# Optimization experiments

Measured on AMD Instinct MI355X. Metric: run time of the kernel, lower is better.

The kernel has to match this reference:

```python
import jax, jax.numpy as jnp
import numpy as np

B = 8192   # batch
N = 1024   # input feature dim
D = 64     # rotation dimension
K = D * (D - 1) // 2  # 2016 upper-triangular entries


def setup_inputs() -> dict:
    key = jax.random.key(0)
    k1, k2 = jax.random.split(key, 2)
    x = jax.random.normal(k1, (B, N), dtype=jnp.float32)
    # nn.Linear(N, K) parameters (kaiming-uniform-ish scale)
    W = jax.random.normal(k2, (K, N), dtype=jnp.float32) / np.float32(np.sqrt(N))
    b = jnp.zeros((K,), dtype=jnp.float32)
    return {"x": x, "W": W, "b": b}


def _skew_expm(A):
    # A is real skew-symmetric => iA is Hermitian: iA = V diag(w) V^H, w real.
    # Hence expm(A) = V diag(exp(-i w)) V^H, which is real orthogonal.
    # Mathematically identical to torch.linalg.matrix_exp(A).
    w, V = jnp.linalg.eigh(1j * A)              # complex64 eigh, batched
    R = jnp.einsum('bij,bj,bkj->bik', V, jnp.exp(-1j * w), V.conj())
    return jnp.real(R)


def reference(x, W, b):
    v = jax.nn.silu(x) @ W.T + b                # (B, K)
    iu, ju = jnp.triu_indices(D, k=1)           # strict upper triangle
    A = jnp.zeros((x.shape[0], D, D), v.dtype)
    A = A.at[:, iu, ju].set(v)
    A = A.at[:, ju, iu].set(-v)                 # skew-symmetric
    return _skew_expm(A)                        # (B, D, D)
```

## Files before the change

### kernel.cpp

```cpp
#include <hip/hip_runtime.h>
#include <hip/hip_bf16.h>
#include <hip/hip_fp16.h>
#include <math.h>

#define BB 8192
#define NF 1024
#define KKc 2016
#define DD 64

typedef unsigned short u16;
typedef __attribute__((ext_vector_type(4))) float f32x4;
typedef __attribute__((ext_vector_type(4))) unsigned int u32x4;
typedef __attribute__((ext_vector_type(8))) short s16x8;
typedef __attribute__((ext_vector_type(8))) _Float16 f16x8;
typedef __attribute__((ext_vector_type(8))) unsigned short u16x8;

union BF2U { __hip_bfloat162 b; unsigned u; };
union H2U { __half2 h; unsigned u; };
union F16U { s16x8 s; f16x8 h; };

__device__ __forceinline__ unsigned pk_hi(float a, float b, float& fa, float& fb) {
  BF2U r; r.b = __float22bfloat162_rn(make_float2(a, b));
  float2 f = __bfloat1622float2(r.b);
  fa = f.x; fb = f.y;
  return r.u;
}
__device__ __forceinline__ unsigned pk(float a, float b) {
  BF2U r; r.b = __float22bfloat162_rn(make_float2(a, b));
  return r.u;
}
__device__ __forceinline__ unsigned pkh(float a, float b) {
  H2U r; r.h = __float22half2_rn(make_float2(a, b));
  return r.u;
}

__device__ __forceinline__ void split4(const float t0, const float t1, const float t2,
                                       const float t3, uint2& h, uint2& l) {
  float f0, f1, f2, f3;
  h.x = pk_hi(t0, t1, f0, f1);
  h.y = pk_hi(t2, t3, f2, f3);
  l.x = pk(t0 - f0, t1 - f1);
  l.y = pk(t2 - f2, t3 - f3);
}

__global__ __launch_bounds__(256)
void prep_f16_kernel(const float* __restrict__ x, const float* __restrict__ W,
                     u16* __restrict__ xf, u16* __restrict__ wfp) {
  const int bid = blockIdx.x;
  if (bid < BB) {
    const int idx = bid * 256 + threadIdx.x;
    float4 vv = ((const float4*)x)[idx];
    float a[4] = {vv.x, vv.y, vv.z, vv.w};
#pragma unroll
    for (int i = 0; i < 4; i++) a[i] = a[i] / (1.f + __expf(-a[i]));
    uint2 o;
    o.x = pkh(a[0], a[1]);
    o.y = pkh(a[2], a[3]);
    ((uint2*)xf)[idx] = o;
  } else {
    const int idx = (bid - BB) * 256 + threadIdx.x;
    const int row = idx >> 8;
    float4 vv = make_float4(0.f, 0.f, 0.f, 0.f);
    if (row < KKc) vv = ((const float4*)W)[idx];
    uint2 o;
    o.x = pkh(vv.x, vv.y);
    o.y = pkh(vv.z, vv.w);
    ((uint2*)wfp)[idx] = o;
  }
}

typedef __attribute__((address_space(1))) const unsigned int gu32;
typedef __attribute__((address_space(3))) unsigned int lu32;

__device__ __forceinline__ void gload_lds16(const void* g, void* l) {
  __builtin_amdgcn_global_load_lds((gu32*)g, (lu32*)l, 16, 0, 0);
}

__device__ __forceinline__ s16x8 frag_row32(const u16* T, int row, int kc) {
  const int c = kc ^ ((row >> 1) & 3);
  return *(const s16x8*)(T + row * 32 + c * 8);
}

__global__ __launch_bounds__(256, 4)
void gemm_f16_kernel(const u16* __restrict__ xf, const u16* __restrict__ wfp,
                     const float* __restrict__ bias, float* __restrict__ v) {
  __shared__ __align__(16) u16 Af[128 * 32];
  __shared__ __align__(16) u16 Bf[128 * 32];
  const int tid = threadIdx.x;
  const int l = tid & 63, w = tid >> 6;
  const int wi = w >> 1, wj = w & 1;
  const int lin = (blockIdx.x & 7) * 128 + (blockIdx.x >> 3);
  const int n0 = (lin & 15) * 128;
  const int m0 = (lin >> 4) * 128;
  const int kc = l >> 4, lr = l & 15;

  const u16* P = (w < 2) ? xf : wfp;
  u16* T = (w < 2) ? Af : Bf;
  const int row0 = ((w < 2) ? m0 : n0) + (w & 1) * 64;
  u16* Th = T + (w & 1) * 2048;

  f32x4 acc[4][4];
  const f32x4 zz = {0.f, 0.f, 0.f, 0.f};
#pragma unroll
  for (int a = 0; a < 4; a++)
#pragma unroll
    for (int b = 0; b < 4; b++) acc[a][b] = zz;

  for (int k0 = 0; k0 < NF; k0 += 32) {
#pragma unroll
    for (int c4 = 0; c4 < 4; c4++) {
      const int slot = c4 * 64 + l;
      const int r = slot >> 2;
      const int c = (slot & 3) ^ ((r >> 1) & 3);
      gload_lds16(P + (size_t)(row0 + r) * NF + k0 + c * 8, Th + c4 * 512);
    }
    __syncthreads();

    F16U fa[4], fb[4];
#pragma unroll
    for (int a = 0; a < 4; a++) fa[a].s = frag_row32(Af, wi * 64 + a * 16 + lr, kc);
#pragma unroll
    for (int b = 0; b < 4; b++) fb[b].s = frag_row32(Bf, wj * 64 + b * 16 + lr, kc);
#pragma unroll
    for (int b = 0; b < 4; b++)
#pragma unroll
      for (int a = 0; a < 4; a++)
        acc[a][b] = __builtin_amdgcn_mfma_f32_16x16x32_f16(fa[a].h, fb[b].h, acc[a][b], 0, 0, 0);
    __syncthreads();
  }

  const int grp = l >> 4;
#pragma unroll
  for (int b = 0; b < 4; b++) {
    const int n = n0 + wj * 64 + b * 16 + lr;
    if (n < KKc) {
      const float bb = bias[n];
#pragma unroll
      for (int a = 0; a < 4; a++) {
        const int mbase = m0 + wi * 64 + a * 16 + grp * 4;
#pragma unroll
        for (int i = 0; i < 4; i++)
          v[(size_t)(mbase + i) * KKc + n] = acc[a][b][i] + bb;
      }
    }
  }
}

#define BM 128
#define BN 128
#define BKr 16
#define XST 132

__global__ __launch_bounds__(256, 2)
void gemm_silu_kernel(const float* __restrict__ x, const float* __restrict__ W,
                      const float* __restrict__ bias, float* __restrict__ v) {
  __shared__ float xs[BKr * XST];
  __shared__ float wl[BKr * XST];
  const int tid = threadIdx.x;
  const int tx = tid & 15, ty = tid >> 4;
  const int c0g = blockIdx.x * BN;
  const int m0 = blockIdx.y * BM;
  const int lrow = tid >> 2;
  const int lu = (tid & 3) << 2;

  float acc[2][2][4][4];
#pragma unroll
  for (int a = 0; a < 2; a++)
#pragma unroll
    for (int b = 0; b < 2; b++)
#pragma unroll
      for (int i = 0; i < 4; i++)
#pragma unroll
        for (int j = 0; j < 4; j++) acc[a][b][i][j] = 0.f;

  for (int n0 = 0; n0 < NF; n0 += BKr) {
#pragma unroll
    for (int p = 0; p < 2; p++) {
      const int row = lrow + 64 * p;
      float4 xv = *(const float4*)(x + (size_t)(m0 + row) * NF + n0 + lu);
      float xa[4] = {xv.x, xv.y, xv.z, xv.w};
#pragma unroll
      for (int u = 0; u < 4; u++) {
        const float val = xa[u];
        xs[(lu + u) * XST + row] = val / (1.f + __expf(-val));
      }
      const int wr = c0g + row;
      float4 wv = make_float4(0.f, 0.f, 0.f, 0.f);
      if (wr < KKc) wv = *(const float4*)(W + (size_t)wr * NF + n0 + lu);
      float wa[4] = {wv.x, wv.y, wv.z, wv.w};
#pragma unroll
      for (int u = 0; u < 4; u++) wl[(lu + u) * XST + row] = wa[u];
    }
    __syncthreads();
#pragma unroll
    for (int k0 = 0; k0 < BKr; k0 += 4) {
#pragma unroll
      for (int kk = 0; kk < 4; kk++) {
        const float* xr = xs + (k0 + kk) * XST;
        const float* wr_ = wl + (k0 + kk) * XST;
        float4 t;
        t = *(const float4*)(xr + 4 * ty);       float a0[4] = {t.x, t.y, t.z, t.w};
        t = *(const float4*)(xr + 64 + 4 * ty);  float a1[4] = {t.x, t.y, t.z, t.w};
        t = *(const float4*)(wr_ + 4 * tx);      float b0[4] = {t.x, t.y, t.z, t.w};
        t = *(const float4*)(wr_ + 64 + 4 * tx); float b1[4] = {t.x, t.y, t.z, t.w};
#pragma unroll
        for (int i = 0; i < 4; i++)
#pragma unroll
          for (int j = 0; j < 4; j++) {
            acc[0][0][i][j] = fmaf(a0[i], b0[j], acc[0][0][i][j]);
            acc[0][1][i][j] = fmaf(a0[i], b1[j], acc[0][1][i][j]);
            acc[1][0][i][j] = fmaf(a1[i], b0[j], acc[1][0][i][j]);
            acc[1][1][i][j] = fmaf(a1[i], b1[j], acc[1][1][i][j]);
          }
      }
    }
    __syncthreads();
  }
#pragma unroll
  for (int rb = 0; rb < 2; rb++)
#pragma unroll
    for (int ii = 0; ii < 4; ii++) {
      const int row = m0 + rb * 64 + 4 * ty + ii;
#pragma unroll
      for (int cb = 0; cb < 2; cb++) {
        const int c = c0g + cb * 64 + 4 * tx;
        if (c < KKc) {
          float4 bb = *(const float4*)(bias + c);
          float4 o;
          o.x = acc[rb][cb][ii][0] + bb.x;
          o.y = acc[rb][cb][ii][1] + bb.y;
          o.z = acc[rb][cb][ii][2] + bb.z;
          o.w = acc[rb][cb][ii][3] + bb.w;
          *(float4*)(v + (size_t)row * KKc + c) = o;
        }
      }
    }
}


__device__ __forceinline__ s16x8 fragld(const u16* P, int row, int chunk) {
  return *(const s16x8*)(P + ((row << 6) | ((chunk ^ (row & 7)) << 3)));
}

__device__ __forceinline__ void mat_mm3(const u16* APh, const u16* APl,
                                        const u16* BPh, const u16* BPl,
                                        f32x4 acc[2][2], int wi, int wj, int g, int lr) {
#pragma unroll
  for (int kb = 0; kb < 2; kb++) {
    const int ch = (kb << 2) | g;
    s16x8 bh[2], bl[2];
#pragma unroll
    for (int b = 0; b < 2; b++) {
      const int n = wj * 32 + b * 16 + lr;
      bh[b] = fragld(BPh, n, ch);
      bl[b] = fragld(BPl, n, ch);
    }
#pragma unroll
    for (int a = 0; a < 2; a++) {
      const int r = wi * 32 + a * 16 + lr;
      const s16x8 ah = fragld(APh, r, ch);
      const s16x8 al = fragld(APl, r, ch);
#pragma unroll
      for (int b = 0; b < 2; b++) {
        acc[a][b] = __builtin_amdgcn_mfma_f32_16x16x32_bf16(ah, bh[b], acc[a][b], 0, 0, 0);
        acc[a][b] = __builtin_amdgcn_mfma_f32_16x16x32_bf16(ah, bl[b], acc[a][b], 0, 0, 0);
        acc[a][b] = __builtin_amdgcn_mfma_f32_16x16x32_bf16(al, bh[b], acc[a][b], 0, 0, 0);
      }
    }
  }
}

__device__ __forceinline__ void mat_mm1h(const u16* AP, const u16* BP,
                                         f32x4 acc[2][2], int wi, int wj, int g, int lr) {
#pragma unroll
  for (int kb = 0; kb < 2; kb++) {
    const int ch = (kb << 2) | g;
    F16U bh[2];
#pragma unroll
    for (int b = 0; b < 2; b++) bh[b].s = fragld(BP, wj * 32 + b * 16 + lr, ch);
#pragma unroll
    for (int a = 0; a < 2; a++) {
      F16U ah; ah.s = fragld(AP, wi * 32 + a * 16 + lr, ch);
#pragma unroll
      for (int b = 0; b < 2; b++)
        acc[a][b] = __builtin_amdgcn_mfma_f32_16x16x32_f16(ah.h, bh[b].h, acc[a][b], 0, 0, 0);
    }
  }
}

__device__ __forceinline__ void pack_col(u16* Ch, u16* Cl, const f32x4 acc[2][2],
                                         int wi, int wj, int g, int lr) {
#pragma unroll
  for (int a = 0; a < 2; a++) {
    const int r0 = wi * 32 + a * 16 + g * 4;
#pragma unroll
    for (int b = 0; b < 2; b++) {
      const int c = wj * 32 + b * 16 + lr;
      uint2 h, l;
      split4(acc[a][b][0], acc[a][b][1], acc[a][b][2], acc[a][b][3], h, l);
      const int ad = (c << 6) | (((((r0 >> 3)) ^ (c & 7)) << 3) | (r0 & 7));
      *(uint2*)(Ch + ad) = h;
      *(uint2*)(Cl + ad) = l;
    }
  }
}

__device__ __forceinline__ void pack_colh(u16* C, const f32x4 acc[2][2], float sc,
                                          int wi, int wj, int g, int lr) {
#pragma unroll
  for (int a = 0; a < 2; a++) {
    const int r0 = wi * 32 + a * 16 + g * 4;
#pragma unroll
    for (int b = 0; b < 2; b++) {
      const int c = wj * 32 + b * 16 + lr;
      uint2 h;
      h.x = pkh(sc * acc[a][b][0], sc * acc[a][b][1]);
      h.y = pkh(sc * acc[a][b][2], sc * acc[a][b][3]);
      const int ad = (c << 6) | (((((r0 >> 3)) ^ (c & 7)) << 3) | (r0 & 7));
      *(uint2*)(C + ad) = h;
    }
  }
}

__device__ __forceinline__ void pack_dualh(u16* Rrow, u16* Rcol, const f32x4 acc[2][2],
                                           int wi, int wj, int g, int lr) {
#pragma unroll
  for (int a = 0; a < 2; a++) {
    const int r0 = wi * 32 + a * 16 + g * 4;
#pragma unroll
    for (int b = 0; b < 2; b++) {
      const int c = wj * 32 + b * 16 + lr;
      uint2 h;
      h.x = pkh(acc[a][b][0], acc[a][b][1]);
      h.y = pkh(acc[a][b][2], acc[a][b][3]);
      const int adc = (c << 6) | (((((r0 >> 3)) ^ (c & 7)) << 3) | (r0 & 7));
      *(uint2*)(Rcol + adc) = h;
      const u16 hv[4] = {(u16)h.x, (u16)(h.x >> 16), (u16)h.y, (u16)(h.y >> 16)};
#pragma unroll
      for (int i = 0; i < 4; i++) {
        const int r = r0 + i;
        const int adr = (r << 6) | ((((c >> 3) ^ (r & 7)) << 3) | (c & 7));
        Rrow[adr] = hv[i];
      }
    }
  }
}

__global__ __launch_bounds__(256, 4)
void expm_kernel(const float* __restrict__ v, float* __restrict__ out) {
  __shared__ __align__(16) u16 P0[4096], P1[4096];
  __shared__ __align__(16) u16 P2[4096], P3[4096];
  __shared__ float red[4];
  const int tid = threadIdx.x;
  const int bid = blockIdx.x;
  const int l = tid & 63, w = tid >> 6;
  const int g = l >> 4, lr = l & 15;
  const int wi = w >> 1, wj = w & 1;

  {
    const float* vr = v + (size_t)bid * KKc;
    const int arow = tid >> 2, q = tid & 3;
    const int ub = (arow * (127 - arow)) / 2 - arow - 1;
    const int c0 = q * 16;
    int il = (c0 * (127 - c0)) / 2 + arow - c0 - 1;
    float va[16];
#pragma unroll
    for (int j = 0; j < 16; j++) {
      const int c = c0 + j;
      float val = 0.f;
      if (arow < c)      val =  vr[ub + c];
      else if (arow > c) val = -vr[il];
      va[j] = val;
      il += 62 - c;
    }
#pragma unroll
    for (int cc = 0; cc < 2; cc++) {
      const int ch = 2 * q + cc;
      const int ad = (arow << 6) | ((ch ^ (arow & 7)) << 3);
      unsigned hw[4], lw[4], fw[4];
#pragma unroll
      for (int p = 0; p < 4; p++) {
        const float a = va[cc * 8 + 2 * p], b = va[cc * 8 + 2 * p + 1];
        float fa, fb;
        hw[p] = pk_hi(a, b, fa, fb);
        lw[p] = pk(a - fa, b - fb);
        fw[p] = pkh(a, b);
      }
      *(u32x4*)(P0 + ad) = (u32x4){hw[0], hw[1], hw[2], hw[3]};
      *(u32x4*)(P1 + ad) = (u32x4){lw[0], lw[1], lw[2], lw[3]};
      *(u32x4*)(P3 + ad) = (u32x4){fw[0], fw[1], fw[2], fw[3]};
    }
  }
  __syncthreads();

  const f32x4 zz = {0.f, 0.f, 0.f, 0.f};
  f32x4 acc[2][2];

  acc[0][0] = zz; acc[0][1] = zz; acc[1][0] = zz; acc[1][1] = zz;
  mat_mm1h(P3, P3, acc, wi, wj, g, lr);
  f32x4 rM[2][2];
  rM[0][0] = acc[0][0]; rM[0][1] = acc[0][1]; rM[1][0] = acc[1][0]; rM[1][1] = acc[1][1];
  pack_colh(P2, rM, -0.0625f, wi, wj, g, lr);
  __syncthreads();

  acc[0][0] = zz; acc[0][1] = zz; acc[1][0] = zz; acc[1][1] = zz;
  mat_mm1h(P2, P2, acc, wi, wj, g, lr);
  {
    float fs = 0.f;
#pragma unroll
    for (int a = 0; a < 2; a++)
#pragma unroll
      for (int b = 0; b < 2; b++)
#pragma unroll
        for (int i = 0; i < 4; i++) fs = fmaf(acc[a][b][i], acc[a][b][i], fs);
#pragma unroll
    for (int k = 1; k < 64; k <<= 1) fs += __shfl_xor(fs, k, 64);
    if (l == 0) red[w] = fs;
  }
  pack_colh(P3, acc, 1.f, wi, wj, g, lr);
  __syncthreads();

  const float nf8 = red[0] + red[1] + red[2] + red[3];
  int s = 0;
  if (nf8 > 1e-30f) {
    s = (int)ceilf(1.0f + 0.125f * log2f(nf8));
    if (s < 0) s = 0;
    if (s > 15) s = 15;
  }
  const float t = exp2f(-(float)s);
  const float t2 = t * t, t4 = t2 * t2, t6 = t4 * t2, t8 = t4 * t4;
  const float e2 = 0.5f * t2,            e4 = 256.f * t4 / 24.f;
  const float e6 = 4096.f * t6 / 720.f,  e8 = 65536.f * t8 / 40320.f;
  const float o1 = t,                    o3 = t * t2 / 6.f;
  const float o5 = 256.f * t * t4 / 120.f, o7 = 4096.f * t * t6 / 5040.f;
  const float o9 = 65536.f * t * t8 / 362880.f;

  f32x4 rE[2][2], rS3[2][2];
#pragma unroll
  for (int a = 0; a < 2; a++)
#pragma unroll
    for (int b = 0; b < 2; b++)
#pragma unroll
      for (int i = 0; i < 4; i++) {
        const int row = wi * 32 + a * 16 + g * 4 + i;
        const int col = wj * 32 + b * 16 + lr;
        const float dg = (row == col) ? 1.f : 0.f;
        rE[a][b][i]  = dg - e2 * rM[a][b][i] + e4 * acc[a][b][i];
        rS3[a][b][i] = o1 * dg - o3 * rM[a][b][i] + o5 * acc[a][b][i];
      }

  acc[0][0] = zz; acc[0][1] = zz; acc[1][0] = zz; acc[1][1] = zz;
  mat_mm1h(P3, P2, acc, wi, wj, g, lr);
#pragma unroll
  for (int a = 0; a < 2; a++)
#pragma unroll
    for (int b = 0; b < 2; b++)
#pragma unroll
      for (int i = 0; i < 4; i++) {
        rE[a][b][i]  += e6 * acc[a][b][i];
        rS3[a][b][i] += o7 * acc[a][b][i];
      }
  acc[0][0] = zz; acc[0][1] = zz; acc[1][0] = zz; acc[1][1] = zz;
  mat_mm1h(P3, P3, acc, wi, wj, g, lr);
#pragma unroll
  for (int a = 0; a < 2; a++)
#pragma unroll
    for (int b = 0; b < 2; b++)
#pragma unroll
      for (int i = 0; i < 4; i++) {
        rE[a][b][i]  += e8 * acc[a][b][i];
        rS3[a][b][i] += o9 * acc[a][b][i];
      }
  __syncthreads();

  pack_col(P2, P3, rS3, wi, wj, g, lr);
  __syncthreads();

  acc[0][0] = rE[0][0]; acc[0][1] = rE[0][1]; acc[1][0] = rE[1][0]; acc[1][1] = rE[1][1];
  mat_mm3(P0, P1, P2, P3, acc, wi, wj, g, lr);
  __syncthreads();

  for (int it = 0; it < s; it++) {
    u16* Rrow = (it & 1) ? P3 : P1;
    u16* Rcol = (it & 1) ? P2 : P0;
    pack_dualh(Rrow, Rcol, acc, wi, wj, g, lr);
    __syncthreads();
    acc[0][0] = zz; acc[0][1] = zz; acc[1][0] = zz; acc[1][1] = zz;
    mat_mm1h(Rrow, Rcol, acc, wi, wj, g, lr);
  }

  float* ob = out + (size_t)bid * 4096;
#pragma unroll
  for (int a = 0; a < 2; a++)
#pragma unroll
    for (int b = 0; b < 2; b++)
#pragma unroll
      for (int i = 0; i < 4; i++) {
        const int row = wi * 32 + a * 16 + g * 4 + i;
        const int col = wj * 32 + b * 16 + lr;
        ob[row * 64 + col] = acc[a][b][i];
      }
}

extern "C" void kernel_launch(void* const* d_in, const int* in_sizes, int n_in,
                              void* d_out, int out_size, void* d_ws, size_t ws_size,
                              hipStream_t stream) {
  const float* x = (const float*)d_in[0];
  const float* W = (const float*)d_in[1];
  const float* bias = (const float*)d_in[2];
  float* out = (float*)d_out;
  char* ws = (char*)d_ws;
  float* v = (float*)ws;

  const size_t V_BYTES  = (size_t)BB * KKc * 4;
  const size_t XF_ELEMS = (size_t)BB * NF;
  const size_t WF_ELEMS = (size_t)2048 * NF;
  const size_t NEED = V_BYTES + (XF_ELEMS + WF_ELEMS) * 2;

  if (ws_size >= NEED) {
    u16* xf = (u16*)(ws + V_BYTES);
    u16* wfp = xf + XF_ELEMS;
    prep_f16_kernel<<<dim3(BB + 2048), dim3(256), 0, stream>>>(x, W, xf, wfp);
    gemm_f16_kernel<<<dim3(1024), dim3(256), 0, stream>>>(xf, wfp, bias, v);
  } else {
    dim3 g1((KKc + BN - 1) / BN, BB / BM);
    gemm_silu_kernel<<<g1, dim3(256), 0, stream>>>(x, W, bias, v);
  }
  expm_kernel<<<dim3(BB), dim3(256), 0, stream>>>(v, out);
}
```

Measured before the change: 167.1 us.

## Track matrix and its transpose during squaring to vectorize stores

The squaring phase now keeps both R and its transpose in registers, each computed by its own MFMA product. This replaces the scattered scalar row-layout LDS writes with column-packed vector writes. Storing the transposed accumulator lets the final output go out as float4 stores instead of scalar ones. The cost is roughly double the matrix multiplies per squaring step (the last step skips one) and more register pressure.

```diff
diff --git a/kernel.cpp b/kernel.cpp
--- a/kernel.cpp
+++ b/kernel.cpp
@@ -322,30 +322,6 @@
   }
 }
 
-__device__ __forceinline__ void pack_dualh(u16* Rrow, u16* Rcol, const f32x4 acc[2][2],
-                                           int wi, int wj, int g, int lr) {
-#pragma unroll
-  for (int a = 0; a < 2; a++) {
-    const int r0 = wi * 32 + a * 16 + g * 4;
-#pragma unroll
-    for (int b = 0; b < 2; b++) {
-      const int c = wj * 32 + b * 16 + lr;
-      uint2 h;
-      h.x = pkh(acc[a][b][0], acc[a][b][1]);
-      h.y = pkh(acc[a][b][2], acc[a][b][3]);
-      const int adc = (c << 6) | (((((r0 >> 3)) ^ (c & 7)) << 3) | (r0 & 7));
-      *(uint2*)(Rcol + adc) = h;
-      const u16 hv[4] = {(u16)h.x, (u16)(h.x >> 16), (u16)h.y, (u16)(h.y >> 16)};
-#pragma unroll
-      for (int i = 0; i < 4; i++) {
-        const int r = r0 + i;
-        const int adr = (r << 6) | ((((c >> 3) ^ (r & 7)) << 3) | (c & 7));
-        Rrow[adr] = hv[i];
-      }
-    }
-  }
-}
-
 __global__ __launch_bounds__(256, 4)
 void expm_kernel(const float* __restrict__ v, float* __restrict__ out) {
   __shared__ __align__(16) u16 P0[4096], P1[4096];
@@ -476,30 +452,38 @@
   pack_col(P2, P3, rS3, wi, wj, g, lr);
   __syncthreads();
 
+  f32x4 accT[2][2];
   acc[0][0] = rE[0][0]; acc[0][1] = rE[0][1]; acc[1][0] = rE[1][0]; acc[1][1] = rE[1][1];
+  accT[0][0] = rE[0][0]; accT[0][1] = rE[0][1]; accT[1][0] = rE[1][0]; accT[1][1] = rE[1][1];
   mat_mm3(P0, P1, P2, P3, acc, wi, wj, g, lr);
+  mat_mm3(P2, P3, P0, P1, accT, wi, wj, g, lr);
   __syncthreads();
 
   for (int it = 0; it < s; it++) {
-    u16* Rrow = (it & 1) ? P3 : P1;
-    u16* Rcol = (it & 1) ? P2 : P0;
-    pack_dualh(Rrow, Rcol, acc, wi, wj, g, lr);
+    u16* Pcol = (it & 1) ? P2 : P0;
+    u16* Prow = (it & 1) ? P3 : P1;
+    pack_colh(Pcol, acc, 1.f, wi, wj, g, lr);
+    pack_colh(Prow, accT, 1.f, wi, wj, g, lr);
     __syncthreads();
-    acc[0][0] = zz; acc[0][1] = zz; acc[1][0] = zz; acc[1][1] = zz;
-    mat_mm1h(Rrow, Rcol, acc, wi, wj, g, lr);
+    accT[0][0] = zz; accT[0][1] = zz; accT[1][0] = zz; accT[1][1] = zz;
+    mat_mm1h(Pcol, Prow, accT, wi, wj, g, lr);
+    if (it < s - 1) {
+      acc[0][0] = zz; acc[0][1] = zz; acc[1][0] = zz; acc[1][1] = zz;
+      mat_mm1h(Prow, Pcol, acc, wi, wj, g, lr);
+    }
   }
 
   float* ob = out + (size_t)bid * 4096;
 #pragma unroll
-  for (int a = 0; a < 2; a++)
-#pragma unroll
-    for (int b = 0; b < 2; b++)
-#pragma unroll
-      for (int i = 0; i < 4; i++) {
-        const int row = wi * 32 + a * 16 + g * 4 + i;
-        const int col = wj * 32 + b * 16 + lr;
-        ob[row * 64 + col] = acc[a][b][i];
-      }
+  for (int a = 0; a < 2; a++) {
+    const int rt0 = wi * 32 + a * 16 + g * 4;
+#pragma unroll
+    for (int b = 0; b < 2; b++) {
+      const int ct = wj * 32 + b * 16 + lr;
+      *(float4*)(ob + ct * 64 + rt0) =
+          make_float4(accT[a][b][0], accT[a][b][1], accT[a][b][2], accT[a][b][3]);
+    }
+  }
 }
 
 extern "C" void kernel_launch(void* const* d_in, const int* in_sizes, int n_in,
```

Result: slower. 175.3 us (+4.9%).

## Split expm work across eight waves per matrix instead of four

Applied to the files above, without the earlier changes.

The expm kernel now launches 512 threads per 64x64 matrix, and each wave owns a 16x32 output tile instead of 32x32. All MFMA helpers, the pack routines, the load stage and the norm reduction are rewritten for two accumulators per wave. The aim is more waves to hide LDS and MFMA latency and fewer registers per thread. In exchange, each wave reuses its fragments less, so LDS fragment loads per MFMA rise, and block-wide barriers now synchronise more waves.

```diff
diff --git a/kernel.cpp b/kernel.cpp
--- a/kernel.cpp
+++ b/kernel.cpp
@@ -244,113 +244,93 @@
 
 __device__ __forceinline__ void mat_mm3(const u16* APh, const u16* APl,
                                         const u16* BPh, const u16* BPl,
-                                        f32x4 acc[2][2], int wi, int wj, int g, int lr) {
+                                        f32x4 acc[2], int wi, int wj, int g, int lr) {
 #pragma unroll
   for (int kb = 0; kb < 2; kb++) {
     const int ch = (kb << 2) | g;
-    s16x8 bh[2], bl[2];
+    const int r = wi * 16 + lr;
+    const s16x8 ah = fragld(APh, r, ch);
+    const s16x8 al = fragld(APl, r, ch);
 #pragma unroll
     for (int b = 0; b < 2; b++) {
       const int n = wj * 32 + b * 16 + lr;
-      bh[b] = fragld(BPh, n, ch);
-      bl[b] = fragld(BPl, n, ch);
-    }
-#pragma unroll
-    for (int a = 0; a < 2; a++) {
-      const int r = wi * 32 + a * 16 + lr;
-      const s16x8 ah = fragld(APh, r, ch);
-      const s16x8 al = fragld(APl, r, ch);
-#pragma unroll
-      for (int b = 0; b < 2; b++) {
-        acc[a][b] = __builtin_amdgcn_mfma_f32_16x16x32_bf16(ah, bh[b], acc[a][b], 0, 0, 0);
-        acc[a][b] = __builtin_amdgcn_mfma_f32_16x16x32_bf16(ah, bl[b], acc[a][b], 0, 0, 0);
-        acc[a][b] = __builtin_amdgcn_mfma_f32_16x16x32_bf16(al, bh[b], acc[a][b], 0, 0, 0);
-      }
+      const s16x8 bh = fragld(BPh, n, ch);
+      const s16x8 bl = fragld(BPl, n, ch);
+      acc[b] = __builtin_amdgcn_mfma_f32_16x16x32_bf16(ah, bh, acc[b], 0, 0, 0);
+      acc[b] = __builtin_amdgcn_mfma_f32_16x16x32_bf16(ah, bl, acc[b], 0, 0, 0);
+      acc[b] = __builtin_amdgcn_mfma_f32_16x16x32_bf16(al, bh, acc[b], 0, 0, 0);
     }
   }
 }
 
 __device__ __forceinline__ void mat_mm1h(const u16* AP, const u16* BP,
-                                         f32x4 acc[2][2], int wi, int wj, int g, int lr) {
+                                         f32x4 acc[2], int wi, int wj, int g, int lr) {
 #pragma unroll
   for (int kb = 0; kb < 2; kb++) {
     const int ch = (kb << 2) | g;
-    F16U bh[2];
-#pragma unroll
-    for (int b = 0; b < 2; b++) bh[b].s = fragld(BP, wj * 32 + b * 16 + lr, ch);
-#pragma unroll
-    for (int a = 0; a < 2; a++) {
-      F16U ah; ah.s = fragld(AP, wi * 32 + a * 16 + lr, ch);
-#pragma unroll
-      for (int b = 0; b < 2; b++)
-        acc[a][b] = __builtin_amdgcn_mfma_f32_16x16x32_f16(ah.h, bh[b].h, acc[a][b], 0, 0, 0);
-    }
-  }
-}
-
-__device__ __forceinline__ void pack_col(u16* Ch, u16* Cl, const f32x4 acc[2][2],
+    F16U ah; ah.s = fragld(AP, wi * 16 + lr, ch);
+#pragma unroll
+    for (int b = 0; b < 2; b++) {
+      F16U bh; bh.s = fragld(BP, wj * 32 + b * 16 + lr, ch);
+      acc[b] = __builtin_amdgcn_mfma_f32_16x16x32_f16(ah.h, bh.h, acc[b], 0, 0, 0);
+    }
+  }
+}
+
+__device__ __forceinline__ void pack_col(u16* Ch, u16* Cl, const f32x4 acc[2],
                                          int wi, int wj, int g, int lr) {
-#pragma unroll
-  for (int a = 0; a < 2; a++) {
-    const int r0 = wi * 32 + a * 16 + g * 4;
-#pragma unroll
-    for (int b = 0; b < 2; b++) {
-      const int c = wj * 32 + b * 16 + lr;
-      uint2 h, l;
-      split4(acc[a][b][0], acc[a][b][1], acc[a][b][2], acc[a][b][3], h, l);
-      const int ad = (c << 6) | (((((r0 >> 3)) ^ (c & 7)) << 3) | (r0 & 7));
-      *(uint2*)(Ch + ad) = h;
-      *(uint2*)(Cl + ad) = l;
-    }
-  }
-}
-
-__device__ __forceinline__ void pack_colh(u16* C, const f32x4 acc[2][2], float sc,
+  const int r0 = wi * 16 + g * 4;
+#pragma unroll
+  for (int b = 0; b < 2; b++) {
+    const int c = wj * 32 + b * 16 + lr;
+    uint2 h, l;
+    split4(acc[b][0], acc[b][1], acc[b][2], acc[b][3], h, l);
+    const int ad = (c << 6) | (((((r0 >> 3)) ^ (c & 7)) << 3) | (r0 & 7));
+    *(uint2*)(Ch + ad) = h;
+    *(uint2*)(Cl + ad) = l;
+  }
+}
+
+__device__ __forceinline__ void pack_colh(u16* C, const f32x4 acc[2], float sc,
                                           int wi, int wj, int g, int lr) {
-#pragma unroll
-  for (int a = 0; a < 2; a++) {
-    const int r0 = wi * 32 + a * 16 + g * 4;
-#pragma unroll
-    for (int b = 0; b < 2; b++) {
-      const int c = wj * 32 + b * 16 + lr;
-      uint2 h;
-      h.x = pkh(sc * acc[a][b][0], sc * acc[a][b][1]);
-      h.y = pkh(sc * acc[a][b][2], sc * acc[a][b][3]);
-      const int ad = (c << 6) | (((((r0 >> 3)) ^ (c & 7)) << 3) | (r0 & 7));
-      *(uint2*)(C + ad) = h;
-    }
-  }
-}
-
-__device__ __forceinline__ void pack_dualh(u16* Rrow, u16* Rcol, const f32x4 acc[2][2],
+  const int r0 = wi * 16 + g * 4;
+#pragma unroll
+  for (int b = 0; b < 2; b++) {
+    const int c = wj * 32 + b * 16 + lr;
+    uint2 h;
+    h.x = pkh(sc * acc[b][0], sc * acc[b][1]);
+    h.y = pkh(sc * acc[b][2], sc * acc[b][3]);
+    const int ad = (c << 6) | (((((r0 >> 3)) ^ (c & 7)) << 3) | (r0 & 7));
+    *(uint2*)(C + ad) = h;
+  }
+}
+
+__device__ __forceinline__ void pack_dualh(u16* Rrow, u16* Rcol, const f32x4 acc[2],
                                            int wi, int wj, int g, int lr) {
-#pragma unroll
-  for (int a = 0; a < 2; a++) {
-    const int r0 = wi * 32 + a * 16 + g * 4;
-#pragma unroll
-    for (int b = 0; b < 2; b++) {
-      const int c = wj * 32 + b * 16 + lr;
-      uint2 h;
-      h.x = pkh(acc[a][b][0], acc[a][b][1]);
-      h.y = pkh(acc[a][b][2], acc[a][b][3]);
-      const int adc = (c << 6) | (((((r0 >> 3)) ^ (c & 7)) << 3) | (r0 & 7));
-      *(uint2*)(Rcol + adc) = h;
-      const u16 hv[4] = {(u16)h.x, (u16)(h.x >> 16), (u16)h.y, (u16)(h.y >> 16)};
-#pragma unroll
-      for (int i = 0; i < 4; i++) {
-        const int r = r0 + i;
-        const int adr = (r << 6) | ((((c >> 3) ^ (r & 7)) << 3) | (c & 7));
-        Rrow[adr] = hv[i];
-      }
-    }
-  }
-}
-
-__global__ __launch_bounds__(256, 4)
+  const int r0 = wi * 16 + g * 4;
+#pragma unroll
+  for (int b = 0; b < 2; b++) {
+    const int c = wj * 32 + b * 16 + lr;
+    uint2 h;
+    h.x = pkh(acc[b][0], acc[b][1]);
+    h.y = pkh(acc[b][2], acc[b][3]);
+    const int adc = (c << 6) | (((((r0 >> 3)) ^ (c & 7)) << 3) | (r0 & 7));
+    *(uint2*)(Rcol + adc) = h;
+    const u16 hv[4] = {(u16)h.x, (u16)(h.x >> 16), (u16)h.y, (u16)(h.y >> 16)};
+#pragma unroll
+    for (int i = 0; i < 4; i++) {
+      const int r = r0 + i;
+      const int adr = (r << 6) | ((((c >> 3) ^ (r & 7)) << 3) | (c & 7));
+      Rrow[adr] = hv[i];
+    }
+  }
+}
+
+__global__ __launch_bounds__(512, 8)
 void expm_kernel(const float* __restrict__ v, float* __restrict__ out) {
   __shared__ __align__(16) u16 P0[4096], P1[4096];
   __shared__ __align__(16) u16 P2[4096], P3[4096];
-  __shared__ float red[4];
+  __shared__ float red[8];
   const int tid = threadIdx.x;
   const int bid = blockIdx.x;
   const int l = tid & 63, w = tid >> 6;
@@ -359,13 +339,13 @@
 
   {
     const float* vr = v + (size_t)bid * KKc;
-    const int arow = tid >> 2, q = tid & 3;
+    const int arow = tid >> 3, q = tid & 7;
     const int ub = (arow * (127 - arow)) / 2 - arow - 1;
-    const int c0 = q * 16;
+    const int c0 = q * 8;
     int il = (c0 * (127 - c0)) / 2 + arow - c0 - 1;
-    float va[16];
-#pragma unroll
-    for (int j = 0; j < 16; j++) {
+    float va[8];
+#pragma unroll
+    for (int j = 0; j < 8; j++) {
       const int c = c0 + j;
       float val = 0.f;
       if (arow < c)      val =  vr[ub + c];
@@ -373,46 +353,40 @@
       va[j] = val;
       il += 62 - c;
     }
-#pragma unroll
-    for (int cc = 0; cc < 2; cc++) {
-      const int ch = 2 * q + cc;
-      const int ad = (arow << 6) | ((ch ^ (arow & 7)) << 3);
-      unsigned hw[4], lw[4], fw[4];
-#pragma unroll
-      for (int p = 0; p < 4; p++) {
-        const float a = va[cc * 8 + 2 * p], b = va[cc * 8 + 2 * p + 1];
-        float fa, fb;
-        hw[p] = pk_hi(a, b, fa, fb);
-        lw[p] = pk(a - fa, b - fb);
-        fw[p] = pkh(a, b);
-      }
-      *(u32x4*)(P0 + ad) = (u32x4){hw[0], hw[1], hw[2], hw[3]};
-      *(u32x4*)(P1 + ad) = (u32x4){lw[0], lw[1], lw[2], lw[3]};
-      *(u32x4*)(P3 + ad) = (u32x4){fw[0], fw[1], fw[2], fw[3]};
-    }
+    const int ad = (arow << 6) | ((q ^ (arow & 7)) << 3);
+    unsigned hw[4], lw[4], fw[4];
+#pragma unroll
+    for (int p = 0; p < 4; p++) {
+      const float a = va[2 * p], b = va[2 * p + 1];
+      float fa, fb;
+      hw[p] = pk_hi(a, b, fa, fb);
+      lw[p] = pk(a - fa, b - fb);
+      fw[p] = pkh(a, b);
+    }
+    *(u32x4*)(P0 + ad) = (u32x4){hw[0], hw[1], hw[2], hw[3]};
+    *(u32x4*)(P1 + ad) = (u32x4){lw[0], lw[1], lw[2], lw[3]};
+    *(u32x4*)(P3 + ad) = (u32x4){fw[0], fw[1], fw[2], fw[3]};
   }
   __syncthreads();
 
   const f32x4 zz = {0.f, 0.f, 0.f, 0.f};
-  f32x4 acc[2][2];
-
-  acc[0][0] = zz; acc[0][1] = zz; acc[1][0] = zz; acc[1][1] = zz;
+  f32x4 acc[2];
+
+  acc[0] = zz; acc[1] = zz;
   mat_mm1h(P3, P3, acc, wi, wj, g, lr);
-  f32x4 rM[2][2];
-  rM[0][0] = acc[0][0]; rM[0][1] = acc[0][1]; rM[1][0] = acc[1][0]; rM[1][1] = acc[1][1];
+  f32x4 rM[2];
+  rM[0] = acc[0]; rM[1] = acc[1];
   pack_colh(P2, rM, -0.0625f, wi, wj, g, lr);
   __syncthreads();
 
-  acc[0][0] = zz; acc[0][1] = zz; acc[1][0] = zz; acc[1][1] = zz;
+  acc[0] = zz; acc[1] = zz;
   mat_mm1h(P2, P2, acc, wi, wj, g, lr);
   {
     float fs = 0.f;
 #pragma unroll
-    for (int a = 0; a < 2; a++)
-#pragma unroll
-      for (int b = 0; b < 2; b++)
-#pragma unroll
-        for (int i = 0; i < 4; i++) fs = fmaf(acc[a][b][i], acc[a][b][i], fs);
+    for (int b = 0; b < 2; b++)
+#pragma unroll
+      for (int i = 0; i < 4; i++) fs = fmaf(acc[b][i], acc[b][i], fs);
 #pragma unroll
     for (int k = 1; k < 64; k <<= 1) fs += __shfl_xor(fs, k, 64);
     if (l == 0) red[w] = fs;
@@ -420,7 +394,7 @@
   pack_colh(P3, acc, 1.f, wi, wj, g, lr);
   __syncthreads();
 
-  const float nf8 = red[0] + red[1] + red[2] + red[3];
+  const float nf8 = red[0] + red[1] + red[2] + red[3] + red[4] + red[5] + red[6] + red[7];
   int s = 0;
   if (nf8 > 1e-30f) {
     s = (int)ceilf(1.0f + 0.125f * log2f(nf8));
@@ -435,48 +409,42 @@
   const float o5 = 256.f * t * t4 / 120.f, o7 = 4096.f * t * t6 / 5040.f;
   const float o9 = 65536.f * t * t8 / 362880.f;
 
-  f32x4 rE[2][2], rS3[2][2];
-#pragma unroll
-  for (int a = 0; a < 2; a++)
-#pragma unroll
-    for (int b = 0; b < 2; b++)
-#pragma unroll
-      for (int i = 0; i < 4; i++) {
-        const int row = wi * 32 + a * 16 + g * 4 + i;
-        const int col = wj * 32 + b * 16 + lr;
-        const float dg = (row == col) ? 1.f : 0.f;
-        rE[a][b][i]  = dg - e2 * rM[a][b][i] + e4 * acc[a][b][i];
-        rS3[a][b][i] = o1 * dg - o3 * rM[a][b][i] + o5 * acc[a][b][i];
-      }
-
-  acc[0][0] = zz; acc[0][1] = zz; acc[1][0] = zz; acc[1][1] = zz;
+  f32x4 rE[2], rS3[2];
+#pragma unroll
+  for (int b = 0; b < 2; b++)
+#pragma unroll
+    for (int i = 0; i < 4; i++) {
+      const int row = wi * 16 + g * 4 + i;
+      const int col = wj * 32 + b * 16 + lr;
+      const float dg = (row == col) ? 1.f : 0.f;
+      rE[b][i]  = dg - e2 * rM[b][i] + e4 * acc[b][i];
+      rS3[b][i] = o1 * dg - o3 * rM[b][i] + o5 * acc[b][i];
+    }
+
+  acc[0] = zz; acc[1] = zz;
   mat_mm1h(P3, P2, acc, wi, wj, g, lr);
 #pragma unroll
-  for (int a = 0; a < 2; a++)
-#pragma unroll
-    for (int b = 0; b < 2; b++)
-#pragma unroll
-      for (int i = 0; i < 4; i++) {
-        rE[a][b][i]  += e6 * acc[a][b][i];
-        rS3[a][b][i] += o7 * acc[a][b][i];
-      }
-  acc[0][0] = zz; acc[0][1] = zz; acc[1][0] = zz; acc[1][1] = zz;
+  for (int b = 0; b < 2; b++)
+#pragma unroll
+    for (int i = 0; i < 4; i++) {
+      rE[b][i]  += e6 * acc[b][i];
+      rS3[b][i] += o7 * acc[b][i];
+    }
+  acc[0] = zz; acc[1] = zz;
   mat_mm1h(P3, P3, acc, wi, wj, g, lr);
 #pragma unroll
-  for (int a = 0; a < 2; a++)
-#pragma unroll
-    for (int b = 0; b < 2; b++)
-#pragma unroll
-      for (int i = 0; i < 4; i++) {
-        rE[a][b][i]  += e8 * acc[a][b][i];
-        rS3[a][b][i] += o9 * acc[a][b][i];
-      }
+  for (int b = 0; b < 2; b++)
+#pragma unroll
+    for (int i = 0; i < 4; i++) {
+      rE[b][i]  += e8 * acc[b][i];
+      rS3[b][i] += o9 * acc[b][i];
+    }
   __syncthreads();
 
   pack_col(P2, P3, rS3, wi, wj, g, lr);
   __syncthreads();
 
-  acc[0][0] = rE[0][0]; acc[0][1] = rE[0][1]; acc[1][0] = rE[1][0]; acc[1][1] = rE[1][1];
+  acc[0] = rE[0]; acc[1] = rE[1];
   mat_mm3(P0, P1, P2, P3, acc, wi, wj, g, lr);
   __syncthreads();
 
@@ -485,21 +453,19 @@
     u16* Rcol = (it & 1) ? P2 : P0;
     pack_dualh(Rrow, Rcol, acc, wi, wj, g, lr);
     __syncthreads();
-    acc[0][0] = zz; acc[0][1] = zz; acc[1][0] = zz; acc[1][1] = zz;
+    acc[0] = zz; acc[1] = zz;
     mat_mm1h(Rrow, Rcol, acc, wi, wj, g, lr);
   }
 
   float* ob = out + (size_t)bid * 4096;
 #pragma unroll
-  for (int a = 0; a < 2; a++)
-#pragma unroll
-    for (int b = 0; b < 2; b++)
-#pragma unroll
-      for (int i = 0; i < 4; i++) {
-        const int row = wi * 32 + a * 16 + g * 4 + i;
-        const int col = wj * 32 + b * 16 + lr;
-        ob[row * 64 + col] = acc[a][b][i];
-      }
+  for (int b = 0; b < 2; b++)
+#pragma unroll
+    for (int i = 0; i < 4; i++) {
+      const int row = wi * 16 + g * 4 + i;
+      const int col = wj * 32 + b * 16 + lr;
+      ob[row * 64 + col] = acc[b][i];
+    }
 }
 
 extern "C" void kernel_launch(void* const* d_in, const int* in_sizes, int n_in,
@@ -526,5 +492,5 @@
     dim3 g1((KKc + BN - 1) / BN, BB / BM);
     gemm_silu_kernel<<<g1, dim3(256), 0, stream>>>(x, W, bias, v);
   }
-  expm_kernel<<<dim3(BB), dim3(256), 0, stream>>>(v, out);
-}
+  expm_kernel<<<dim3(BB), dim3(512), 0, stream>>>(v, out);
+}
```

After: 176.0 us. 1.05x slower.
